# Optimization experiments

Measured on AMD Instinct MI355X. Metric: run time of the kernel, lower is better.

## Reference

```python
import jax, jax.numpy as jnp
import numpy as np

B, T, C, H = 2, 2048, 1024, 16
D = C // H  # head dim = 64
NEG_MIN = jnp.finfo(jnp.float32).min


def setup_inputs() -> dict:
    key = jax.random.key(0)
    ks = jax.random.split(key, 5)
    std = 0.02
    return {
        "x": jax.random.normal(ks[0], (B, T, C), dtype=jnp.float32),
        "Wq": std * jax.random.normal(ks[1], (C, C), dtype=jnp.float32),
        "bq": jnp.zeros((C,), dtype=jnp.float32),
        "Wk": std * jax.random.normal(ks[2], (C, C), dtype=jnp.float32),
        "bk": jnp.zeros((C,), dtype=jnp.float32),
        "Wv": std * jax.random.normal(ks[3], (C, C), dtype=jnp.float32),
        "bv": jnp.zeros((C,), dtype=jnp.float32),
        "Wo": (std / np.sqrt(24.0)) * jax.random.normal(ks[4], (C, C), dtype=jnp.float32),
        "bo": jnp.zeros((C,), dtype=jnp.float32),
    }


def reference(x, Wq, bq, Wk, bk, Wv, bv, Wo, bo):
    # QKV projections -> (B, H, T, D)
    def proj(W, b):
        return (x @ W + b).reshape(B, T, H, D).transpose(0, 2, 1, 3)

    q = proj(Wq, bq)
    k = proj(Wk, bk)
    v = proj(Wv, bv)

    # full scores (B, H, T, T), causal mask, softmax
    attn = jnp.einsum("bhqd,bhkd->bhqk", q, k) / jnp.sqrt(jnp.float32(D))
    mask = jnp.tril(jnp.ones((T, T), dtype=bool))[None, None]
    attn = jnp.where(mask, attn, NEG_MIN)
    scores = jax.nn.softmax(attn, axis=-1)

    out = jnp.einsum("bhqk,bhkd->bhqd", scores, v)
    out = out.transpose(0, 2, 1, 3).reshape(B, T, C)
    return out @ Wo + bo
```

## Files before the change

kernel.cpp:

```cpp
#include <hip/hip_runtime.h>
#include <stdint.h>
#include <stddef.h>


#define B_SZ 2
#define T_SZ 2048
#define C_SZ 1024
#define H_SZ 16
#define D_SZ 64
#define M_SZ (B_SZ * T_SZ)
#define BHTD (B_SZ * H_SZ * T_SZ * D_SZ)
#define CC (C_SZ * C_SZ)

typedef __attribute__((ext_vector_type(8))) __bf16 bf16x8;
typedef __attribute__((ext_vector_type(4))) float f32x4;
typedef __attribute__((ext_vector_type(16))) float f32x16;

__device__ __forceinline__ unsigned short f2bf(float f) {
    union { float f; unsigned u; } v; v.f = f;
    v.u += 0x7fffu + ((v.u >> 16) & 1u);
    return (unsigned short)(v.u >> 16);
}

__device__ __forceinline__ unsigned pkbf(float lo, float hi_) {
    union { unsigned u; __bf16 h[2]; } r;
    r.h[0] = (__bf16)lo; r.h[1] = (__bf16)hi_;
    return r.u;
}

__device__ __forceinline__ void load_lds16(const unsigned short* g, unsigned short* l) {
    __builtin_amdgcn_global_load_lds(
        (const __attribute__((address_space(1))) void*)g,
        (__attribute__((address_space(3))) void*)l, 16, 0, 0);
}


__global__ void cvt_x_kernel(const float4* __restrict__ in, ushort4* __restrict__ out, int n4) {
    int stride = gridDim.x * blockDim.x;
    for (int i = blockIdx.x * blockDim.x + threadIdx.x; i < n4; i += stride) {
        float4 v = in[i];
        ushort4 o;
        o.x = f2bf(v.x); o.y = f2bf(v.y); o.z = f2bf(v.z); o.w = f2bf(v.w);
        out[i] = o;
    }
}

__global__ __launch_bounds__(256) void transpose_cvt_kernel(
    const float* __restrict__ W0, const float* __restrict__ W1,
    const float* __restrict__ W2, const float* __restrict__ W3,
    unsigned short* __restrict__ T0, unsigned short* __restrict__ T1,
    unsigned short* __restrict__ T2, unsigned short* __restrict__ T3)
{
    __shared__ float tile[32][33];
    const float* W; unsigned short* Wt;
    switch (blockIdx.z) {
        case 0: W = W0; Wt = T0; break;
        case 1: W = W1; Wt = T1; break;
        case 2: W = W2; Wt = T2; break;
        default: W = W3; Wt = T3; break;
    }
    const int tx = threadIdx.x, ty = threadIdx.y;
    const int n0 = blockIdx.x * 32, k0 = blockIdx.y * 32;
    #pragma unroll
    for (int i = 0; i < 4; i++)
        tile[ty + i * 8][tx] = W[(size_t)(k0 + ty + i * 8) * C_SZ + n0 + tx];
    __syncthreads();
    #pragma unroll
    for (int i = 0; i < 4; i++)
        Wt[(size_t)(n0 + ty + i * 8) * C_SZ + k0 + tx] = f2bf(tile[tx][ty + i * 8]);
}

__global__ __launch_bounds__(256) void vt_kernel(
    const unsigned short* __restrict__ V, unsigned short* __restrict__ Vt)
{
    __shared__ unsigned short tile[32][33];
    const int bh = blockIdx.z;
    const int t0 = blockIdx.x * 32, d0 = blockIdx.y * 32;
    const unsigned short* src = V + (size_t)bh * T_SZ * D_SZ;
    unsigned short* dst = Vt + (size_t)bh * T_SZ * D_SZ;
    const int tx = threadIdx.x, ty = threadIdx.y;
    #pragma unroll
    for (int i = 0; i < 4; i++)
        tile[ty + i * 8][tx] = src[(size_t)(t0 + ty + i * 8) * D_SZ + d0 + tx];
    __syncthreads();
    #pragma unroll
    for (int i = 0; i < 4; i++)
        dst[(size_t)(d0 + ty + i * 8) * T_SZ + t0 + tx] = tile[tx][ty + i * 8];
}


__device__ __forceinline__ void gemm_tile_core(
    const unsigned short* __restrict__ A,
    const unsigned short* __restrict__ Bt,
    unsigned short* As, unsigned short* Bs,
    int m0, int n0, f32x4 acc[4][4])
{
    const int tid = threadIdx.x;
    const int lane = tid & 63;
    const int w = tid >> 6;
    const int l15 = lane & 15, lg = lane >> 4;
    const int wr = (w >> 1) * 64, wc = (w & 1) * 64;

    const unsigned short* Ag0 = A + (size_t)(m0 + (tid >> 2)) * C_SZ + (tid & 3) * 8;
    const unsigned short* Ag1 = Ag0 + (size_t)64 * C_SZ;
    const unsigned short* Bg0 = Bt + (size_t)(n0 + (tid >> 2)) * C_SZ + (tid & 3) * 8;
    const unsigned short* Bg1 = Bg0 + (size_t)64 * C_SZ;
    unsigned short* As0 = As + w * 512;
    unsigned short* As1 = As + 2048 + w * 512;
    unsigned short* Bs0 = Bs + w * 512;
    unsigned short* Bs1 = Bs + 2048 + w * 512;

    for (int k0 = 0; k0 < C_SZ; k0 += 32) {
        load_lds16(Ag0 + k0, As0);
        load_lds16(Ag1 + k0, As1);
        load_lds16(Bg0 + k0, Bs0);
        load_lds16(Bg1 + k0, Bs1);
        __syncthreads();
        bf16x8 af[4], bfv[4];
        const bf16x8* Ap = (const bf16x8*)As;
        const bf16x8* Bp = (const bf16x8*)Bs;
        #pragma unroll
        for (int m = 0; m < 4; m++) af[m] = Ap[(wr + m * 16 + l15) * 4 + lg];
        #pragma unroll
        for (int n = 0; n < 4; n++) bfv[n] = Bp[(wc + n * 16 + l15) * 4 + lg];
        #pragma unroll
        for (int m = 0; m < 4; m++)
            #pragma unroll
            for (int n = 0; n < 4; n++)
                acc[m][n] = __builtin_amdgcn_mfma_f32_16x16x32_bf16(af[m], bfv[n], acc[m][n], 0, 0, 0);
        __syncthreads();
    }
}

__global__ __launch_bounds__(256) void gemm_qkv_kernel(
    const unsigned short* __restrict__ A,
    const unsigned short* __restrict__ WtBase,
    const float* __restrict__ bq, const float* __restrict__ bk, const float* __restrict__ bv,
    unsigned short* __restrict__ QKV, unsigned short* __restrict__ Vtmp)
{
    __shared__ unsigned short As[4096], Bs[4096];
    const int z = blockIdx.z;
    const unsigned short* Bt = WtBase + (size_t)z * CC;
    const float* bias = (z == 0) ? bq : (z == 1) ? bk : bv;
    const float scale = (z == 0) ? 0.18033688011112042f : 1.0f;
    unsigned short* Out = (z == 2) ? Vtmp : QKV + (size_t)z * BHTD;

    f32x4 acc[4][4];
    f32x4 zero4 = {0.f, 0.f, 0.f, 0.f};
    #pragma unroll
    for (int m = 0; m < 4; m++)
        #pragma unroll
        for (int n = 0; n < 4; n++) acc[m][n] = zero4;

    const int m0 = blockIdx.y * 128, n0 = blockIdx.x * 128;
    gemm_tile_core(A, Bt, As, Bs, m0, n0, acc);

    const int lane = threadIdx.x & 63;
    const int w = threadIdx.x >> 6;
    const int l15 = lane & 15, lg = lane >> 4;
    const int wr = (w >> 1) * 64, wc = (w & 1) * 64;
    #pragma unroll
    for (int n = 0; n < 4; n++) {
        const int col = n0 + wc + n * 16 + l15;
        const float bias_v = bias[col];
        const int h = col >> 6, d = col & 63;
        #pragma unroll
        for (int m = 0; m < 4; m++) {
            #pragma unroll
            for (int j = 0; j < 4; j++) {
                const int row = m0 + wr + m * 16 + lg * 4 + j;
                const int b = row >> 11, t = row & (T_SZ - 1);
                Out[(((size_t)(b * H_SZ + h)) * T_SZ + t) * D_SZ + d] =
                    f2bf((acc[m][n][j] + bias_v) * scale);
            }
        }
    }
}

__global__ __launch_bounds__(256) void gemm_out_kernel(
    const unsigned short* __restrict__ A,
    const unsigned short* __restrict__ Bt,
    const float* __restrict__ bo,
    float* __restrict__ Out)
{
    __shared__ unsigned short As[4096], Bs[4096];
    f32x4 acc[4][4];
    f32x4 zero4 = {0.f, 0.f, 0.f, 0.f};
    #pragma unroll
    for (int m = 0; m < 4; m++)
        #pragma unroll
        for (int n = 0; n < 4; n++) acc[m][n] = zero4;

    const int m0 = blockIdx.y * 128, n0 = blockIdx.x * 128;
    gemm_tile_core(A, Bt, As, Bs, m0, n0, acc);

    const int lane = threadIdx.x & 63;
    const int w = threadIdx.x >> 6;
    const int l15 = lane & 15, lg = lane >> 4;
    const int wr = (w >> 1) * 64, wc = (w & 1) * 64;
    #pragma unroll
    for (int n = 0; n < 4; n++) {
        const int col = n0 + wc + n * 16 + l15;
        const float bias_v = bo[col];
        #pragma unroll
        for (int m = 0; m < 4; m++) {
            #pragma unroll
            for (int j = 0; j < 4; j++) {
                const int row = m0 + wr + m * 16 + lg * 4 + j;
                Out[(size_t)row * C_SZ + col] = acc[m][n][j] + bias_v;
            }
        }
    }
}

__global__ __launch_bounds__(256) void attn_fwd_kernel(
    const unsigned short* __restrict__ Q,
    const unsigned short* __restrict__ K,
    const unsigned short* __restrict__ Vt,
    unsigned short* __restrict__ O)
{
    const int idx = blockIdx.x;
    const int xcd = idx & 7, jj0 = idx >> 3;
    const int qt = 15 - (jj0 >> 2);
    const int bh = (xcd << 2) | (jj0 & 3);
    const int w = threadIdx.x >> 6;
    const int lane = threadIdx.x & 63;
    const int l31 = lane & 31, hi = lane >> 5;
    const int qw = qt * 128 + 32 * w;

    const unsigned short* Qh = Q + (size_t)bh * T_SZ * D_SZ;
    const unsigned short* Kh = K + (size_t)bh * T_SZ * D_SZ;
    const unsigned short* Vh = Vt + (size_t)bh * T_SZ * D_SZ;

    __shared__ __align__(16) unsigned short smem[9216];
    unsigned short* Ks = smem;
    unsigned short* Vs = smem + 4096;

    const int c0 = w * 64 + lane;
    const int row0 = c0 >> 3;
    const int sw0 = (c0 & 7) ^ (row0 & 7);
    const int koff0 = row0 * 64 + sw0 * 8;
    const int koff1 = koff0 + 2048;
    const int voff0 = row0 * T_SZ + sw0 * 8;
    const int voff1 = voff0 + 32 * T_SZ;
    unsigned short* ldsK0 = Ks + w * 512;
    unsigned short* ldsK1 = Ks + 2048 + w * 512;
    unsigned short* ldsV0 = Vs + w * 512;
    unsigned short* ldsV1 = Vs + 2048 + w * 512;

    bf16x8 qf[4];
    #pragma unroll
    for (int j = 0; j < 4; j++)
        qf[j] = *(const bf16x8*)&Qh[(size_t)(qw + l31) * D_SZ + j * 16 + 8 * hi];

    f32x16 acc[2];
    #pragma unroll
    for (int r = 0; r < 16; r++) { acc[0][r] = 0.f; acc[1][r] = 0.f; }
    float mrun = -3.0e38f, lrun = 0.f;

    const int tlast = (qw + 31) >> 6;
    const int ntb = 2 * qt + 2;
    const int qrow = qw + l31;
    const int swl = l31 & 7;

    for (int tt = 0; tt < ntb; ++tt) {
        const int k0 = tt * 64;
        const unsigned short* Kt = Kh + (size_t)k0 * D_SZ;
        const unsigned short* Vtt = Vh + k0;
        load_lds16(Kt + koff0, ldsK0);
        load_lds16(Kt + koff1, ldsK1);
        load_lds16(Vtt + voff0, ldsV0);
        load_lds16(Vtt + voff1, ldsV1);
        __syncthreads();

        if (tt <= tlast) {
            f32x16 s[2];
            #pragma unroll
            for (int kb = 0; kb < 2; ++kb) {
                bf16x8 kf[4];
                #pragma unroll
                for (int j = 0; j < 4; ++j) {
                    const int ch = (j * 2 + hi) ^ swl;
                    kf[j] = *(const bf16x8*)&Ks[(kb * 32 + l31) * 64 + ch * 8];
                }
                f32x16 sc;
                #pragma unroll
                for (int r = 0; r < 16; r++) sc[r] = 0.f;
                #pragma unroll
                for (int j = 0; j < 4; ++j)
                    sc = __builtin_amdgcn_mfma_f32_32x32x16_bf16(kf[j], qf[j], sc, 0, 0, 0);
                s[kb] = sc;
            }

            if (k0 + 63 > qw) {
                #pragma unroll
                for (int kb = 0; kb < 2; ++kb)
                    #pragma unroll
                    for (int r = 0; r < 16; ++r) {
                        const int kv = k0 + kb * 32 + (r & 3) + 8 * (r >> 2) + 4 * hi;
                        s[kb][r] = (kv > qrow) ? -3.0e38f : s[kb][r];
                    }
            }

            float pm = s[0][0];
            #pragma unroll
            for (int r = 1; r < 16; r++) pm = fmaxf(pm, s[0][r]);
            #pragma unroll
            for (int r = 0; r < 16; r++) pm = fmaxf(pm, s[1][r]);
            pm = fmaxf(pm, __shfl_xor(pm, 32));

            if (!__all(pm <= mrun + 8.0f)) {
                const float mnew = fmaxf(mrun, pm);
                const float al = exp2f(mrun - mnew);
                lrun *= al;
                #pragma unroll
                for (int r = 0; r < 16; r++) { acc[0][r] *= al; acc[1][r] *= al; }
                mrun = mnew;
            }

            float ps = 0.f;
            #pragma unroll
            for (int kb = 0; kb < 2; ++kb)
                #pragma unroll
                for (int r = 0; r < 16; r++) { s[kb][r] = exp2f(s[kb][r] - mrun); ps += s[kb][r]; }
            ps += __shfl_xor(ps, 32);
            lrun += ps;

            bf16x8 pf[2][2];
            #pragma unroll
            for (int kb = 0; kb < 2; ++kb) {
                #pragma unroll
                for (int ksl = 0; ksl < 2; ++ksl) {
                    unsigned a0 = pkbf(s[kb][8 * ksl + 0], s[kb][8 * ksl + 1]);
                    unsigned a1 = pkbf(s[kb][8 * ksl + 2], s[kb][8 * ksl + 3]);
                    unsigned b0 = pkbf(s[kb][8 * ksl + 4], s[kb][8 * ksl + 5]);
                    unsigned b1 = pkbf(s[kb][8 * ksl + 6], s[kb][8 * ksl + 7]);
                    asm volatile("v_permlane32_swap_b32 %0, %1" : "+v"(a0), "+v"(b0));
                    asm volatile("v_permlane32_swap_b32 %0, %1" : "+v"(a1), "+v"(b1));
                    union { unsigned u[4]; bf16x8 v; } fr;
                    fr.u[0] = a0; fr.u[1] = a1; fr.u[2] = b0; fr.u[3] = b1;
                    pf[kb][ksl] = fr.v;
                }
            }

            #pragma unroll
            for (int dt = 0; dt < 2; ++dt)
                #pragma unroll
                for (int kb = 0; kb < 2; ++kb)
                    #pragma unroll
                    for (int ksl = 0; ksl < 2; ++ksl) {
                        const int ks = kb * 2 + ksl;
                        const int ch = (ks * 2 + hi) ^ swl;
                        const bf16x8 vf = *(const bf16x8*)&Vs[(dt * 32 + l31) * 64 + ch * 8];
                        acc[dt] = __builtin_amdgcn_mfma_f32_32x32x16_bf16(vf, pf[kb][ksl], acc[dt], 0, 0, 0);
                    }
        }
        __syncthreads();
    }

    unsigned short* ot = smem + w * 2304;
    const float inv = 1.0f / lrun;
    #pragma unroll
    for (int g = 0; g < 4; g++) {
        ushort4 wa, wb;
        wa.x = f2bf(acc[0][4 * g + 0] * inv); wa.y = f2bf(acc[0][4 * g + 1] * inv);
        wa.z = f2bf(acc[0][4 * g + 2] * inv); wa.w = f2bf(acc[0][4 * g + 3] * inv);
        wb.x = f2bf(acc[1][4 * g + 0] * inv); wb.y = f2bf(acc[1][4 * g + 1] * inv);
        wb.z = f2bf(acc[1][4 * g + 2] * inv); wb.w = f2bf(acc[1][4 * g + 3] * inv);
        *(ushort4*)&ot[l31 * 72 + 8 * g + 4 * hi] = wa;
        *(ushort4*)&ot[l31 * 72 + 32 + 8 * g + 4 * hi] = wb;
    }
    const int b = bh >> 4, h = bh & 15;
    #pragma unroll
    for (int pss = 0; pss < 4; pss++) {
        const int q = pss * 8 + (lane >> 3);
        const uint4 val = *(const uint4*)&ot[q * 72 + (lane & 7) * 8];
        *(uint4*)&O[((size_t)(b * T_SZ + qw + q)) * C_SZ + h * D_SZ + (lane & 7) * 8] = val;
    }
}


extern "C" void kernel_launch(void* const* d_in, const int* in_sizes, int n_in,
                              void* d_out, int out_size, void* d_ws, size_t ws_size,
                              hipStream_t stream)
{
    const float* x  = (const float*)d_in[0];
    const float* Wq = (const float*)d_in[1];
    const float* bq = (const float*)d_in[2];
    const float* Wk = (const float*)d_in[3];
    const float* bk = (const float*)d_in[4];
    const float* Wv = (const float*)d_in[5];
    const float* bv = (const float*)d_in[6];
    const float* Wo = (const float*)d_in[7];
    const float* bo = (const float*)d_in[8];

    uint8_t* ws = (uint8_t*)d_ws;
    unsigned short* XB   = (unsigned short*)(ws);
    unsigned short* WT   = (unsigned short*)(ws + (8u  << 20));
    unsigned short* QKV  = (unsigned short*)(ws + (16u << 20));
    unsigned short* Vtmp = (unsigned short*)(ws + (40u << 20));

    cvt_x_kernel<<<2048, 256, 0, stream>>>((const float4*)x, (ushort4*)XB, M_SZ * C_SZ / 4);
    transpose_cvt_kernel<<<dim3(32, 32, 4), dim3(32, 8), 0, stream>>>(
        Wq, Wk, Wv, Wo, WT, WT + CC, WT + 2 * (size_t)CC, WT + 3 * (size_t)CC);
    gemm_qkv_kernel<<<dim3(8, 32, 3), 256, 0, stream>>>(XB, WT, bq, bk, bv, QKV, Vtmp);
    vt_kernel<<<dim3(64, 2, 32), dim3(32, 8), 0, stream>>>(Vtmp, QKV + 2 * (size_t)BHTD);
    attn_fwd_kernel<<<512, 256, 0, stream>>>(
        QKV, QKV + BHTD, QKV + 2 * (size_t)BHTD, Vtmp);
    gemm_out_kernel<<<dim3(8, 32), 256, 0, stream>>>(Vtmp, WT + 3 * (size_t)CC, bo, (float*)d_out);
}
```

Baseline: 132.6 us.

## Shrink attention blocks to 64 query rows and double-buffer K/V tiles

The attention kernel now runs 2-wave blocks of 64 query rows (1024 blocks of 128 threads) instead of 4-wave blocks of 128 rows. This removes the per-wave idle tiles beyond each wave's causal limit and confines masking to the final tile. K/V tiles are double-buffered in LDS, so the next tile's global-to-LDS copy is issued before computing on the current one, overlapping load latency with MFMA work. Each block stages the full tile with fewer threads and uses more LDS, which may lower occupancy. The unseen epilogue may also assume four waves.

```diff
diff --git a/kernel.cpp b/kernel.cpp
--- a/kernel.cpp
+++ b/kernel.cpp
@@ -213,148 +213,159 @@
     }
 }
 
-__global__ __launch_bounds__(256) void attn_fwd_kernel(
+__global__ __launch_bounds__(128) void attn_fwd_kernel(
     const unsigned short* __restrict__ Q,
     const unsigned short* __restrict__ K,
     const unsigned short* __restrict__ Vt,
     unsigned short* __restrict__ O)
 {
     const int idx = blockIdx.x;
-    const int xcd = idx & 7, jj0 = idx >> 3;
-    const int qt = 15 - (jj0 >> 2);
-    const int bh = (xcd << 2) | (jj0 & 3);
+    const int xcd = idx & 7, j0 = idx >> 3;
+    const int bh = (xcd << 2) | (j0 & 3);
+    const int qi = 31 - (j0 >> 2);
     const int w = threadIdx.x >> 6;
     const int lane = threadIdx.x & 63;
     const int l31 = lane & 31, hi = lane >> 5;
-    const int qw = qt * 128 + 32 * w;
+    const int qw = qi * 64 + 32 * w;
 
     const unsigned short* Qh = Q + (size_t)bh * T_SZ * D_SZ;
     const unsigned short* Kh = K + (size_t)bh * T_SZ * D_SZ;
     const unsigned short* Vh = Vt + (size_t)bh * T_SZ * D_SZ;
 
-    __shared__ __align__(16) unsigned short smem[9216];
-    unsigned short* Ks = smem;
-    unsigned short* Vs = smem + 4096;
-
-    const int c0 = w * 64 + lane;
+    __shared__ __align__(16) unsigned short smem[16384];
+
+    const int c0 = threadIdx.x;
     const int row0 = c0 >> 3;
     const int sw0 = (c0 & 7) ^ (row0 & 7);
     const int koff0 = row0 * 64 + sw0 * 8;
-    const int koff1 = koff0 + 2048;
     const int voff0 = row0 * T_SZ + sw0 * 8;
-    const int voff1 = voff0 + 32 * T_SZ;
-    unsigned short* ldsK0 = Ks + w * 512;
-    unsigned short* ldsK1 = Ks + 2048 + w * 512;
-    unsigned short* ldsV0 = Vs + w * 512;
-    unsigned short* ldsV1 = Vs + 2048 + w * 512;
+    const int ldso0 = w * 512;
+
+    f32x16 acc[2];
+    #pragma unroll
+    for (int r = 0; r < 16; r++) { acc[0][r] = 0.f; acc[1][r] = 0.f; }
+    float mrun = -3.0e38f, lrun = 0.f;
 
     bf16x8 qf[4];
     #pragma unroll
     for (int j = 0; j < 4; j++)
         qf[j] = *(const bf16x8*)&Qh[(size_t)(qw + l31) * D_SZ + j * 16 + 8 * hi];
 
-    f32x16 acc[2];
-    #pragma unroll
-    for (int r = 0; r < 16; r++) { acc[0][r] = 0.f; acc[1][r] = 0.f; }
-    float mrun = -3.0e38f, lrun = 0.f;
-
-    const int tlast = (qw + 31) >> 6;
-    const int ntb = 2 * qt + 2;
+    const int ntb = qi + 1;
     const int qrow = qw + l31;
     const int swl = l31 & 7;
 
+    {
+        const unsigned short* Kt = Kh;
+        const unsigned short* Vtt = Vh;
+        #pragma unroll
+        for (int ii = 0; ii < 4; ii++)
+            load_lds16(Kt + koff0 + ii * 1024, smem + ldso0 + ii * 1024);
+        #pragma unroll
+        for (int ii = 0; ii < 4; ii++)
+            load_lds16(Vtt + voff0 + ii * 16 * T_SZ, smem + 4096 + ldso0 + ii * 1024);
+    }
+    __syncthreads();
+
     for (int tt = 0; tt < ntb; ++tt) {
+        if (tt + 1 < ntb) {
+            const int nb = (tt + 1) & 1;
+            const unsigned short* Kt = Kh + (size_t)(tt + 1) * 64 * D_SZ;
+            const unsigned short* Vtt = Vh + (tt + 1) * 64;
+            unsigned short* Kb = smem + nb * 8192;
+            #pragma unroll
+            for (int ii = 0; ii < 4; ii++)
+                load_lds16(Kt + koff0 + ii * 1024, Kb + ldso0 + ii * 1024);
+            #pragma unroll
+            for (int ii = 0; ii < 4; ii++)
+                load_lds16(Vtt + voff0 + ii * 16 * T_SZ, Kb + 4096 + ldso0 + ii * 1024);
+        }
+
+        const unsigned short* Ks = smem + (tt & 1) * 8192;
+        const unsigned short* Vs = Ks + 4096;
         const int k0 = tt * 64;
-        const unsigned short* Kt = Kh + (size_t)k0 * D_SZ;
-        const unsigned short* Vtt = Vh + k0;
-        load_lds16(Kt + koff0, ldsK0);
-        load_lds16(Kt + koff1, ldsK1);
-        load_lds16(Vtt + voff0, ldsV0);
-        load_lds16(Vtt + voff1, ldsV1);
-        __syncthreads();
-
-        if (tt <= tlast) {
-            f32x16 s[2];
-            #pragma unroll
-            for (int kb = 0; kb < 2; ++kb) {
-                bf16x8 kf[4];
-                #pragma unroll
-                for (int j = 0; j < 4; ++j) {
-                    const int ch = (j * 2 + hi) ^ swl;
-                    kf[j] = *(const bf16x8*)&Ks[(kb * 32 + l31) * 64 + ch * 8];
-                }
-                f32x16 sc;
-                #pragma unroll
-                for (int r = 0; r < 16; r++) sc[r] = 0.f;
-                #pragma unroll
-                for (int j = 0; j < 4; ++j)
-                    sc = __builtin_amdgcn_mfma_f32_32x32x16_bf16(kf[j], qf[j], sc, 0, 0, 0);
-                s[kb] = sc;
+
+        f32x16 s[2];
+        #pragma unroll
+        for (int kb = 0; kb < 2; ++kb) {
+            bf16x8 kf[4];
+            #pragma unroll
+            for (int j = 0; j < 4; ++j) {
+                const int ch = (j * 2 + hi) ^ swl;
+                kf[j] = *(const bf16x8*)&Ks[(kb * 32 + l31) * 64 + ch * 8];
             }
-
-            if (k0 + 63 > qw) {
-                #pragma unroll
-                for (int kb = 0; kb < 2; ++kb)
-                    #pragma unroll
-                    for (int r = 0; r < 16; ++r) {
-                        const int kv = k0 + kb * 32 + (r & 3) + 8 * (r >> 2) + 4 * hi;
-                        s[kb][r] = (kv > qrow) ? -3.0e38f : s[kb][r];
-                    }
-            }
-
-            float pm = s[0][0];
-            #pragma unroll
-            for (int r = 1; r < 16; r++) pm = fmaxf(pm, s[0][r]);
-            #pragma unroll
-            for (int r = 0; r < 16; r++) pm = fmaxf(pm, s[1][r]);
-            pm = fmaxf(pm, __shfl_xor(pm, 32));
-
-            if (!__all(pm <= mrun + 8.0f)) {
-                const float mnew = fmaxf(mrun, pm);
-                const float al = exp2f(mrun - mnew);
-                lrun *= al;
-                #pragma unroll
-                for (int r = 0; r < 16; r++) { acc[0][r] *= al; acc[1][r] *= al; }
-                mrun = mnew;
-            }
-
-            float ps = 0.f;
+            f32x16 sc;
+            #pragma unroll
+            for (int r = 0; r < 16; r++) sc[r] = 0.f;
+            #pragma unroll
+            for (int j = 0; j < 4; ++j)
+                sc = __builtin_amdgcn_mfma_f32_32x32x16_bf16(kf[j], qf[j], sc, 0, 0, 0);
+            s[kb] = sc;
+        }
+
+        if (tt == ntb - 1) {
             #pragma unroll
             for (int kb = 0; kb < 2; ++kb)
                 #pragma unroll
-                for (int r = 0; r < 16; r++) { s[kb][r] = exp2f(s[kb][r] - mrun); ps += s[kb][r]; }
-            ps += __shfl_xor(ps, 32);
-            lrun += ps;
-
-            bf16x8 pf[2][2];
-            #pragma unroll
-            for (int kb = 0; kb < 2; ++kb) {
+                for (int r = 0; r < 16; ++r) {
+                    const int kv = k0 + kb * 32 + (r & 3) + 8 * (r >> 2) + 4 * hi;
+                    s[kb][r] = (kv > qrow) ? -3.0e38f : s[kb][r];
+                }
+        }
+
+        float pm = s[0][0];
+        #pragma unroll
+        for (int r = 1; r < 16; r++) pm = fmaxf(pm, s[0][r]);
+        #pragma unroll
+        for (int r = 0; r < 16; r++) pm = fmaxf(pm, s[1][r]);
+        pm = fmaxf(pm, __shfl_xor(pm, 32));
+
+        if (!__all(pm <= mrun + 8.0f)) {
+            const float mnew = fmaxf(mrun, pm);
+            const float al = exp2f(mrun - mnew);
+            lrun *= al;
+            #pragma unroll
+            for (int r = 0; r < 16; r++) { acc[0][r] *= al; acc[1][r] *= al; }
+            mrun = mnew;
+        }
+
+        float ps = 0.f;
+        #pragma unroll
+        for (int kb = 0; kb < 2; ++kb)
+            #pragma unroll
+            for (int r = 0; r < 16; r++) { s[kb][r] = exp2f(s[kb][r] - mrun); ps += s[kb][r]; }
+        ps += __shfl_xor(ps, 32);
+        lrun += ps;
+
+        bf16x8 pf[2][2];
+        #pragma unroll
+        for (int kb = 0; kb < 2; ++kb) {
+            #pragma unroll
+            for (int ksl = 0; ksl < 2; ++ksl) {
+                unsigned a0 = pkbf(s[kb][8 * ksl + 0], s[kb][8 * ksl + 1]);
+                unsigned a1 = pkbf(s[kb][8 * ksl + 2], s[kb][8 * ksl + 3]);
+                unsigned b0 = pkbf(s[kb][8 * ksl + 4], s[kb][8 * ksl + 5]);
+                unsigned b1 = pkbf(s[kb][8 * ksl + 6], s[kb][8 * ksl + 7]);
+                asm volatile("v_permlane32_swap_b32 %0, %1" : "+v"(a0), "+v"(b0));
+                asm volatile("v_permlane32_swap_b32 %0, %1" : "+v"(a1), "+v"(b1));
+                union { unsigned u[4]; bf16x8 v; } fr;
+                fr.u[0] = a0; fr.u[1] = a1; fr.u[2] = b0; fr.u[3] = b1;
+                pf[kb][ksl] = fr.v;
+            }
+        }
+
+        #pragma unroll
+        for (int dt = 0; dt < 2; ++dt)
+            #pragma unroll
+            for (int kb = 0; kb < 2; ++kb)
                 #pragma unroll
                 for (int ksl = 0; ksl < 2; ++ksl) {
-                    unsigned a0 = pkbf(s[kb][8 * ksl + 0], s[kb][8 * ksl + 1]);
-                    unsigned a1 = pkbf(s[kb][8 * ksl + 2], s[kb][8 * ksl + 3]);
-                    unsigned b0 = pkbf(s[kb][8 * ksl + 4], s[kb][8 * ksl + 5]);
-                    unsigned b1 = pkbf(s[kb][8 * ksl + 6], s[kb][8 * ksl + 7]);
-                    asm volatile("v_permlane32_swap_b32 %0, %1" : "+v"(a0), "+v"(b0));
-                    asm volatile("v_permlane32_swap_b32 %0, %1" : "+v"(a1), "+v"(b1));
-                    union { unsigned u[4]; bf16x8 v; } fr;
-                    fr.u[0] = a0; fr.u[1] = a1; fr.u[2] = b0; fr.u[3] = b1;
-                    pf[kb][ksl] = fr.v;
+                    const int ks = kb * 2 + ksl;
+                    const int ch = (ks * 2 + hi) ^ swl;
+                    const bf16x8 vf = *(const bf16x8*)&Vs[(dt * 32 + l31) * 64 + ch * 8];
+                    acc[dt] = __builtin_amdgcn_mfma_f32_32x32x16_bf16(vf, pf[kb][ksl], acc[dt], 0, 0, 0);
                 }
-            }
-
-            #pragma unroll
-            for (int dt = 0; dt < 2; ++dt)
-                #pragma unroll
-                for (int kb = 0; kb < 2; ++kb)
-                    #pragma unroll
-                    for (int ksl = 0; ksl < 2; ++ksl) {
-                        const int ks = kb * 2 + ksl;
-                        const int ch = (ks * 2 + hi) ^ swl;
-                        const bf16x8 vf = *(const bf16x8*)&Vs[(dt * 32 + l31) * 64 + ch * 8];
-                        acc[dt] = __builtin_amdgcn_mfma_f32_32x32x16_bf16(vf, pf[kb][ksl], acc[dt], 0, 0, 0);
-                    }
-        }
+
         __syncthreads();
     }
 
@@ -405,7 +416,7 @@
         Wq, Wk, Wv, Wo, WT, WT + CC, WT + 2 * (size_t)CC, WT + 3 * (size_t)CC);
     gemm_qkv_kernel<<<dim3(8, 32, 3), 256, 0, stream>>>(XB, WT, bq, bk, bv, QKV, Vtmp);
     vt_kernel<<<dim3(64, 2, 32), dim3(32, 8), 0, stream>>>(Vtmp, QKV + 2 * (size_t)BHTD);
-    attn_fwd_kernel<<<512, 256, 0, stream>>>(
+    attn_fwd_kernel<<<1024, 128, 0, stream>>>(
         QKV, QKV + BHTD, QKV + 2 * (size_t)BHTD, Vtmp);
     gemm_out_kernel<<<dim3(8, 32), 256, 0, stream>>>(Vtmp, WT + 3 * (size_t)CC, bo, (float*)d_out);
 }
```

Measured after the change: 148.2 us. +11.7%, slower.

## Fuse V transpose into QKV GEMM epilogue and double-buffer attention K/V loads

Applied to the files above, without the earlier changes.

The QKV GEMM epilogue now writes V directly in transposed (B,H,D,T) layout with packed 4-element stores, so the separate vt_kernel launch and its extra pass over V go away. The attention kernel gets a two-stage LDS double buffer: the K/V tile for the next iteration is issued before computing the current one, with explicit vmcnt waits and raw barriers in place of __syncthreads. LDS use per block grows from 9216 to 16384 elements, which may reduce occupancy, and correctness now depends on the hand-placed waitcnt counts.

```diff
diff --git a/kernel.cpp b/kernel.cpp
--- a/kernel.cpp
+++ b/kernel.cpp
@@ -68,24 +68,6 @@
     #pragma unroll
     for (int i = 0; i < 4; i++)
         Wt[(size_t)(n0 + ty + i * 8) * C_SZ + k0 + tx] = f2bf(tile[tx][ty + i * 8]);
-}
-
-__global__ __launch_bounds__(256) void vt_kernel(
-    const unsigned short* __restrict__ V, unsigned short* __restrict__ Vt)
-{
-    __shared__ unsigned short tile[32][33];
-    const int bh = blockIdx.z;
-    const int t0 = blockIdx.x * 32, d0 = blockIdx.y * 32;
-    const unsigned short* src = V + (size_t)bh * T_SZ * D_SZ;
-    unsigned short* dst = Vt + (size_t)bh * T_SZ * D_SZ;
-    const int tx = threadIdx.x, ty = threadIdx.y;
-    #pragma unroll
-    for (int i = 0; i < 4; i++)
-        tile[ty + i * 8][tx] = src[(size_t)(t0 + ty + i * 8) * D_SZ + d0 + tx];
-    __syncthreads();
-    #pragma unroll
-    for (int i = 0; i < 4; i++)
-        dst[(size_t)(d0 + ty + i * 8) * T_SZ + t0 + tx] = tile[tx][ty + i * 8];
 }
 
 
@@ -136,14 +118,14 @@
     const unsigned short* __restrict__ A,
     const unsigned short* __restrict__ WtBase,
     const float* __restrict__ bq, const float* __restrict__ bk, const float* __restrict__ bv,
-    unsigned short* __restrict__ QKV, unsigned short* __restrict__ Vtmp)
+    unsigned short* __restrict__ QKV)
 {
     __shared__ unsigned short As[4096], Bs[4096];
     const int z = blockIdx.z;
     const unsigned short* Bt = WtBase + (size_t)z * CC;
     const float* bias = (z == 0) ? bq : (z == 1) ? bk : bv;
     const float scale = (z == 0) ? 0.18033688011112042f : 1.0f;
-    unsigned short* Out = (z == 2) ? Vtmp : QKV + (size_t)z * BHTD;
+    unsigned short* Out = QKV + (size_t)z * BHTD;
 
     f32x4 acc[4][4];
     f32x4 zero4 = {0.f, 0.f, 0.f, 0.f};
@@ -159,19 +141,39 @@
     const int w = threadIdx.x >> 6;
     const int l15 = lane & 15, lg = lane >> 4;
     const int wr = (w >> 1) * 64, wc = (w & 1) * 64;
-    #pragma unroll
-    for (int n = 0; n < 4; n++) {
-        const int col = n0 + wc + n * 16 + l15;
-        const float bias_v = bias[col];
-        const int h = col >> 6, d = col & 63;
-        #pragma unroll
-        for (int m = 0; m < 4; m++) {
-            #pragma unroll
-            for (int j = 0; j < 4; j++) {
-                const int row = m0 + wr + m * 16 + lg * 4 + j;
-                const int b = row >> 11, t = row & (T_SZ - 1);
-                Out[(((size_t)(b * H_SZ + h)) * T_SZ + t) * D_SZ + d] =
-                    f2bf((acc[m][n][j] + bias_v) * scale);
+    if (z == 2) {
+        #pragma unroll
+        for (int n = 0; n < 4; n++) {
+            const int col = n0 + wc + n * 16 + l15;
+            const float bias_v = bias[col];
+            const int h = col >> 6, d = col & 63;
+            #pragma unroll
+            for (int m = 0; m < 4; m++) {
+                const int row0 = m0 + wr + m * 16 + lg * 4;
+                const int b = row0 >> 11, t0 = row0 & (T_SZ - 1);
+                ushort4 pk;
+                pk.x = f2bf(acc[m][n][0] + bias_v);
+                pk.y = f2bf(acc[m][n][1] + bias_v);
+                pk.z = f2bf(acc[m][n][2] + bias_v);
+                pk.w = f2bf(acc[m][n][3] + bias_v);
+                *(ushort4*)&Out[(((size_t)(b * H_SZ + h)) * D_SZ + d) * T_SZ + t0] = pk;
+            }
+        }
+    } else {
+        #pragma unroll
+        for (int n = 0; n < 4; n++) {
+            const int col = n0 + wc + n * 16 + l15;
+            const float bias_v = bias[col];
+            const int h = col >> 6, d = col & 63;
+            #pragma unroll
+            for (int m = 0; m < 4; m++) {
+                #pragma unroll
+                for (int j = 0; j < 4; j++) {
+                    const int row = m0 + wr + m * 16 + lg * 4 + j;
+                    const int b = row >> 11, t = row & (T_SZ - 1);
+                    Out[(((size_t)(b * H_SZ + h)) * T_SZ + t) * D_SZ + d] =
+                        f2bf((acc[m][n][j] + bias_v) * scale);
+                }
             }
         }
     }
@@ -232,21 +234,14 @@
     const unsigned short* Kh = K + (size_t)bh * T_SZ * D_SZ;
     const unsigned short* Vh = Vt + (size_t)bh * T_SZ * D_SZ;
 
-    __shared__ __align__(16) unsigned short smem[9216];
-    unsigned short* Ks = smem;
-    unsigned short* Vs = smem + 4096;
+    __shared__ __align__(16) unsigned short smem[16384];
 
     const int c0 = w * 64 + lane;
     const int row0 = c0 >> 3;
     const int sw0 = (c0 & 7) ^ (row0 & 7);
     const int koff0 = row0 * 64 + sw0 * 8;
-    const int koff1 = koff0 + 2048;
     const int voff0 = row0 * T_SZ + sw0 * 8;
-    const int voff1 = voff0 + 32 * T_SZ;
-    unsigned short* ldsK0 = Ks + w * 512;
-    unsigned short* ldsK1 = Ks + 2048 + w * 512;
-    unsigned short* ldsV0 = Vs + w * 512;
-    unsigned short* ldsV1 = Vs + 2048 + w * 512;
+    const int ldsb0 = w * 512;
 
     bf16x8 qf[4];
     #pragma unroll
@@ -263,17 +258,31 @@
     const int qrow = qw + l31;
     const int swl = l31 & 7;
 
+    load_lds16(Kh + koff0, smem + ldsb0);
+    load_lds16(Kh + koff0 + 2048, smem + 2048 + ldsb0);
+    load_lds16(Vh + voff0, smem + 4096 + ldsb0);
+    load_lds16(Vh + voff0 + 32 * T_SZ, smem + 6144 + ldsb0);
+
     for (int tt = 0; tt < ntb; ++tt) {
-        const int k0 = tt * 64;
-        const unsigned short* Kt = Kh + (size_t)k0 * D_SZ;
-        const unsigned short* Vtt = Vh + k0;
-        load_lds16(Kt + koff0, ldsK0);
-        load_lds16(Kt + koff1, ldsK1);
-        load_lds16(Vtt + voff0, ldsV0);
-        load_lds16(Vtt + voff1, ldsV1);
-        __syncthreads();
+        if (tt + 1 < ntb) {
+            unsigned short* Bd = smem + ((tt + 1) & 1) * 8192;
+            const unsigned short* Kt = Kh + (size_t)(tt + 1) * 64 * D_SZ;
+            const unsigned short* Vtt = Vh + (tt + 1) * 64;
+            load_lds16(Kt + koff0, Bd + ldsb0);
+            load_lds16(Kt + koff0 + 2048, Bd + 2048 + ldsb0);
+            load_lds16(Vtt + voff0, Bd + 4096 + ldsb0);
+            load_lds16(Vtt + voff0 + 32 * T_SZ, Bd + 6144 + ldsb0);
+            asm volatile("s_waitcnt vmcnt(4)" ::: "memory");
+        } else {
+            asm volatile("s_waitcnt vmcnt(0)" ::: "memory");
+        }
+        __builtin_amdgcn_s_barrier();
 
         if (tt <= tlast) {
+            const unsigned short* Ks = smem + (tt & 1) * 8192;
+            const unsigned short* Vs = Ks + 4096;
+            const int k0 = tt * 64;
+
             f32x16 s[2];
             #pragma unroll
             for (int kb = 0; kb < 2; ++kb) {
@@ -355,7 +364,7 @@
                         acc[dt] = __builtin_amdgcn_mfma_f32_32x32x16_bf16(vf, pf[kb][ksl], acc[dt], 0, 0, 0);
                     }
         }
-        __syncthreads();
+        __builtin_amdgcn_s_barrier();
     }
 
     unsigned short* ot = smem + w * 2304;
@@ -395,17 +404,16 @@
     const float* bo = (const float*)d_in[8];
 
     uint8_t* ws = (uint8_t*)d_ws;
-    unsigned short* XB   = (unsigned short*)(ws);
-    unsigned short* WT   = (unsigned short*)(ws + (8u  << 20));
-    unsigned short* QKV  = (unsigned short*)(ws + (16u << 20));
-    unsigned short* Vtmp = (unsigned short*)(ws + (40u << 20));
+    unsigned short* XB  = (unsigned short*)(ws);
+    unsigned short* WT  = (unsigned short*)(ws + (8u  << 20));
+    unsigned short* QKV = (unsigned short*)(ws + (16u << 20));
+    unsigned short* OB  = (unsigned short*)(ws + (40u << 20));
 
     cvt_x_kernel<<<2048, 256, 0, stream>>>((const float4*)x, (ushort4*)XB, M_SZ * C_SZ / 4);
     transpose_cvt_kernel<<<dim3(32, 32, 4), dim3(32, 8), 0, stream>>>(
         Wq, Wk, Wv, Wo, WT, WT + CC, WT + 2 * (size_t)CC, WT + 3 * (size_t)CC);
-    gemm_qkv_kernel<<<dim3(8, 32, 3), 256, 0, stream>>>(XB, WT, bq, bk, bv, QKV, Vtmp);
-    vt_kernel<<<dim3(64, 2, 32), dim3(32, 8), 0, stream>>>(Vtmp, QKV + 2 * (size_t)BHTD);
+    gemm_qkv_kernel<<<dim3(8, 32, 3), 256, 0, stream>>>(XB, WT, bq, bk, bv, QKV);
     attn_fwd_kernel<<<512, 256, 0, stream>>>(
-        QKV, QKV + BHTD, QKV + 2 * (size_t)BHTD, Vtmp);
-    gemm_out_kernel<<<dim3(8, 32), 256, 0, stream>>>(Vtmp, WT + 3 * (size_t)CC, bo, (float*)d_out);
-}
+        QKV, QKV + BHTD, QKV + 2 * (size_t)BHTD, OB);
+    gemm_out_kernel<<<dim3(8, 32), 256, 0, stream>>>(OB, WT + 3 * (size_t)CC, bo, (float*)d_out);
+}
```

Measured after the change: 144.7 us. 9.1% more time.

## Double-buffer K/V tiles in attention and reorder block-to-tile mapping

Applied to the files above, without the earlier changes.

Adds a two-stage LDS double buffer to the attention kernel: the next K/V tile is issued with async global-to-LDS loads before computing on the current one, with explicit vmcnt waits and raw barriers replacing __syncthreads. The goal is to hide global load latency behind the MFMA work. It also replaces the XCD-aware block mapping with a scheme that schedules heavy query tiles first and then light ones. LDS use grows to 32 KB per block, which may reduce occupancy, and dropping the XCD grouping may hurt L2 locality.

```diff
diff --git a/kernel.cpp b/kernel.cpp
--- a/kernel.cpp
+++ b/kernel.cpp
@@ -220,9 +220,8 @@
     unsigned short* __restrict__ O)
 {
     const int idx = blockIdx.x;
-    const int xcd = idx & 7, jj0 = idx >> 3;
-    const int qt = 15 - (jj0 >> 2);
-    const int bh = (xcd << 2) | (jj0 & 3);
+    const int qt = (idx < 256) ? (15 - (idx >> 5)) : ((idx - 256) >> 5);
+    const int bh = idx & 31;
     const int w = threadIdx.x >> 6;
     const int lane = threadIdx.x & 63;
     const int l31 = lane & 31, hi = lane >> 5;
@@ -232,21 +231,14 @@
     const unsigned short* Kh = K + (size_t)bh * T_SZ * D_SZ;
     const unsigned short* Vh = Vt + (size_t)bh * T_SZ * D_SZ;
 
-    __shared__ __align__(16) unsigned short smem[9216];
-    unsigned short* Ks = smem;
-    unsigned short* Vs = smem + 4096;
+    __shared__ __align__(16) unsigned short smem[16384];
 
     const int c0 = w * 64 + lane;
     const int row0 = c0 >> 3;
     const int sw0 = (c0 & 7) ^ (row0 & 7);
     const int koff0 = row0 * 64 + sw0 * 8;
-    const int koff1 = koff0 + 2048;
     const int voff0 = row0 * T_SZ + sw0 * 8;
-    const int voff1 = voff0 + 32 * T_SZ;
-    unsigned short* ldsK0 = Ks + w * 512;
-    unsigned short* ldsK1 = Ks + 2048 + w * 512;
-    unsigned short* ldsV0 = Vs + w * 512;
-    unsigned short* ldsV1 = Vs + 2048 + w * 512;
+    const int ldsb0 = w * 512;
 
     bf16x8 qf[4];
     #pragma unroll
@@ -263,17 +255,31 @@
     const int qrow = qw + l31;
     const int swl = l31 & 7;
 
+    load_lds16(Kh + koff0, smem + ldsb0);
+    load_lds16(Kh + koff0 + 2048, smem + 2048 + ldsb0);
+    load_lds16(Vh + voff0, smem + 4096 + ldsb0);
+    load_lds16(Vh + voff0 + 32 * T_SZ, smem + 6144 + ldsb0);
+
     for (int tt = 0; tt < ntb; ++tt) {
-        const int k0 = tt * 64;
-        const unsigned short* Kt = Kh + (size_t)k0 * D_SZ;
-        const unsigned short* Vtt = Vh + k0;
-        load_lds16(Kt + koff0, ldsK0);
-        load_lds16(Kt + koff1, ldsK1);
-        load_lds16(Vtt + voff0, ldsV0);
-        load_lds16(Vtt + voff1, ldsV1);
-        __syncthreads();
+        if (tt + 1 < ntb) {
+            unsigned short* Bd = smem + ((tt + 1) & 1) * 8192;
+            const unsigned short* Kt = Kh + (size_t)(tt + 1) * 64 * D_SZ;
+            const unsigned short* Vtt = Vh + (tt + 1) * 64;
+            load_lds16(Kt + koff0, Bd + ldsb0);
+            load_lds16(Kt + koff0 + 2048, Bd + 2048 + ldsb0);
+            load_lds16(Vtt + voff0, Bd + 4096 + ldsb0);
+            load_lds16(Vtt + voff0 + 32 * T_SZ, Bd + 6144 + ldsb0);
+            asm volatile("s_waitcnt vmcnt(4)" ::: "memory");
+        } else {
+            asm volatile("s_waitcnt vmcnt(0)" ::: "memory");
+        }
+        __builtin_amdgcn_s_barrier();
 
         if (tt <= tlast) {
+            const unsigned short* Ks = smem + (tt & 1) * 8192;
+            const unsigned short* Vs = Ks + 4096;
+            const int k0 = tt * 64;
+
             f32x16 s[2];
             #pragma unroll
             for (int kb = 0; kb < 2; ++kb) {
@@ -355,7 +361,7 @@
                         acc[dt] = __builtin_amdgcn_mfma_f32_32x32x16_bf16(vf, pf[kb][ksl], acc[dt], 0, 0, 0);
                     }
         }
-        __syncthreads();
+        __builtin_amdgcn_s_barrier();
     }
 
     unsigned short* ot = smem + w * 2304;
```

After: 131.8 us. No clear change (-0.6%).
